# Performance work log

Hardware: AMD Instinct MI355X
Metric: run time of the kernel (lower is better)

## Reference

```python
import jax, jax.numpy as jnp
import numpy as np

C = 1.0                      # Poincare-ball curvature (m.default_c)
SQC = C ** 0.5
EPS = 1e-6


def _norm(x):
    return jnp.maximum(jnp.linalg.norm(x, axis=-1, keepdims=True), EPS)


def _artanh(x):
    return jnp.arctanh(jnp.clip(x, -1.0 + 1e-6, 1.0 - 1e-6))


def mobius_add(x, y):
    # Mobius addition in the Poincare ball of curvature C
    x2 = jnp.sum(x * x, axis=-1, keepdims=True)
    y2 = jnp.sum(y * y, axis=-1, keepdims=True)
    xy = jnp.sum(x * y, axis=-1, keepdims=True)
    num = (1 + 2 * C * xy + C * y2) * x + (1 - C * x2) * y
    den = 1 + 2 * C * xy + C * C * x2 * y2
    return num / jnp.maximum(den, EPS)


def mobius_matvec(x, W):
    # m.matmul(W, x, c): Mobius matrix-vector product, x:[B,Din], W:[Din,Dout]
    mx = x @ W
    xn = _norm(x)
    mxn = _norm(mx)
    return jnp.tanh(mxn / xn * _artanh(SQC * xn)) * mx / (mxn * SQC)


def _log0(x):
    xn = _norm(x)
    return _artanh(SQC * xn) * x / (SQC * xn)


def _exp0(v):
    vn = _norm(v)
    return jnp.tanh(SQC * vn) * v / (SQC * vn)


def m_tanh(x):
    # Mobius pointwise tanh: exp0(tanh(log0(x)))
    return _exp0(jnp.tanh(_log0(x)))


def setup_inputs() -> dict:
    key = jax.random.key(0)
    k1, k2, k3, k4 = jax.random.split(key, 4)
    B, T, E, H = 256, 128, 1024, 1024
    # small scale so points stay well inside the unit Poincare ball
    inp = jax.random.normal(k1, (B, T, E), dtype=jnp.float32) * 0.02
    W_ih = jax.random.normal(k2, (E, H), dtype=jnp.float32) * 0.02
    W_hh = jax.random.normal(k3, (H, H), dtype=jnp.float32) * 0.02
    b_h = jax.random.uniform(k4, (H,), dtype=jnp.float32, minval=-0.01, maxval=0.01)
    return {"inp": inp, "W_ih": W_ih, "W_hh": W_hh, "b_h": b_h}


def reference(inp, W_ih, W_hh, b_h):
    B, T, E = inp.shape
    H = W_hh.shape[0]
    h0 = jnp.zeros((B, H), dtype=inp.dtype)

    def step(h, xt):
        prem = mobius_matvec(xt, W_ih)                       # [B,H]
        hid = mobius_add(mobius_matvec(h, W_hh), b_h[None])  # [B,H]
        h_next = m_tanh(mobius_add(prem, hid))
        return h_next, None

    h_last, _ = jax.lax.scan(step, h0, jnp.swapaxes(inp, 0, 1))  # scan over T
    return h_last
```

## Files before the change

### kernel.cpp

```cpp
#include <hip/hip_runtime.h>

#define EPSF 1e-6f
#define ONEM 0.999999f
#define Bb 256
#define Tt 128
#define Kd 1024

typedef __attribute__((ext_vector_type(8))) short s16x8;
typedef __attribute__((ext_vector_type(4))) short s16x4;
typedef __attribute__((ext_vector_type(4))) float f32x4;
typedef unsigned long long ull;

union PF { ull u; float f[2]; };

__device__ __forceinline__ short f2bf(float f) {
  unsigned u = __float_as_uint(f);
  u += 0x7fffu + ((u >> 16) & 1u);
  return (short)(u >> 16);
}
__device__ __forceinline__ float bf2f(short s) {
  return __uint_as_float(((unsigned)(unsigned short)s) << 16);
}
__device__ __forceinline__ float ftanh(float x) {
  float e = __expf(2.f * x);
  return 1.f - 2.f / (e + 1.f);
}
__device__ __forceinline__ float fatanh(float x) {
  return 0.5f * __logf((1.f + x) / (1.f - x));
}
__device__ __forceinline__ float red16(float v) {
#pragma unroll
  for (int m = 8; m >= 1; m >>= 1) v += __shfl_xor(v, m, 64);
  return v;
}

__device__ __forceinline__ float brsum(float v) {
  __shared__ float sb[4];
#pragma unroll
  for (int m = 32; m >= 1; m >>= 1) v += __shfl_xor(v, m, 64);
  __syncthreads();
  if ((threadIdx.x & 63) == 0) sb[threadIdx.x >> 6] = v;
  __syncthreads();
  return sb[0] + sb[1] + sb[2] + sb[3];
}

__device__ __forceinline__ void gbarR(int* c) {
  __syncthreads();
  if (threadIdx.x == 0) {
    __hip_atomic_fetch_add(c, 1, __ATOMIC_RELAXED, __HIP_MEMORY_SCOPE_AGENT);
    while (__hip_atomic_load(c, __ATOMIC_RELAXED, __HIP_MEMORY_SCOPE_AGENT) < 16)
      __builtin_amdgcn_s_sleep(1);
  }
  __syncthreads();
}

__global__ void wcvt_kernel(const float* __restrict__ W, short* __restrict__ WT) {
  __shared__ float tile[64][65];
  const int k0 = blockIdx.y * 64, n0 = blockIdx.x * 64;
  const int t = threadIdx.x;
#pragma unroll
  for (int i = 0; i < 16; i++) {
    int e = i * 256 + t, r = e >> 6, c = e & 63;
    tile[r][c] = W[(k0 + r) * Kd + n0 + c];
  }
  __syncthreads();
#pragma unroll
  for (int i = 0; i < 16; i++) {
    int e = i * 256 + t, rn = e >> 6, ck = e & 63;
    WT[(n0 + rn) * Kd + k0 + ck] = f2bf(tile[ck][rn]);
  }
}

__global__ void wfrag_kernel(const float* __restrict__ W, short* __restrict__ Wf) {
  const int bid = blockIdx.x;
  const int nn = threadIdx.x & 15, kk = threadIdx.x >> 4;
  const int l = (kk >> 2) * 16 + nn;
  const int jj = (kk & 3) * 2;
  const int nt = bid >> 5, kt = bid & 31;
  const int n = nt * 16 + nn;
  const int k = kt * 32 + (kk >> 2) * 8 + jj;
  unsigned lo = (unsigned)(unsigned short)f2bf(W[(size_t)k * Kd + n]);
  unsigned hi = (unsigned)(unsigned short)f2bf(W[(size_t)(k + 1) * Kd + n]);
  ((unsigned*)Wf)[((size_t)bid * 64 + l) * 4 + (jj >> 1)] = lo | (hi << 16);
}

__global__ void icvt_kernel(const float* __restrict__ inp, short* __restrict__ out) {
  int i = blockIdx.x * 2048 + threadIdx.x * 8;
  float4 a = *(const float4*)(inp + i);
  float4 b = *(const float4*)(inp + i + 4);
  s16x8 v;
  v[0] = f2bf(a.x); v[1] = f2bf(a.y); v[2] = f2bf(a.z); v[3] = f2bf(a.w);
  v[4] = f2bf(b.x); v[5] = f2bf(b.y); v[6] = f2bf(b.z); v[7] = f2bf(b.w);
  *(s16x8*)(out + i) = v;
}

__global__ void __launch_bounds__(256) gemm_p_kernel(const short* __restrict__ A,
                                                     const short* __restrict__ BT,
                                                     short* __restrict__ C) {
  const int n0 = blockIdx.x * 64, m0 = blockIdx.y * 64;
  const int tid = threadIdx.x, w = tid >> 6, l = tid & 63, lm = l & 15, q = l >> 4;
  const short* ap = A + (m0 + w * 16 + lm) * Kd + q * 8;
  const short* bp = BT + (n0 + lm) * Kd + q * 8;
  f32x4 acc0 = {0.f, 0.f, 0.f, 0.f}, acc1 = acc0, acc2 = acc0, acc3 = acc0;
#pragma unroll 4
  for (int k = 0; k < Kd; k += 32) {
    s16x8 a = *(const s16x8*)(ap + k);
    s16x8 b0 = *(const s16x8*)(bp + k);
    s16x8 b1 = *(const s16x8*)(bp + 16 * Kd + k);
    s16x8 b2 = *(const s16x8*)(bp + 32 * Kd + k);
    s16x8 b3 = *(const s16x8*)(bp + 48 * Kd + k);
    acc0 = __builtin_amdgcn_mfma_f32_16x16x32_bf16(a, b0, acc0, 0, 0, 0);
    acc1 = __builtin_amdgcn_mfma_f32_16x16x32_bf16(a, b1, acc1, 0, 0, 0);
    acc2 = __builtin_amdgcn_mfma_f32_16x16x32_bf16(a, b2, acc2, 0, 0, 0);
    acc3 = __builtin_amdgcn_mfma_f32_16x16x32_bf16(a, b3, acc3, 0, 0, 0);
  }
  const int row = m0 + w * 16 + q * 4, col = n0 + lm;
#pragma unroll
  for (int r = 0; r < 4; r++) {
    C[(row + r) * Kd + col] = f2bf(acc0[r]);
    C[(row + r) * Kd + col + 16] = f2bf(acc1[r]);
    C[(row + r) * Kd + col + 32] = f2bf(acc2[r]);
    C[(row + r) * Kd + col + 48] = f2bf(acc3[r]);
  }
}

__global__ void __launch_bounds__(256) rowscale_kernel(const float* __restrict__ inp,
                                                       const float* __restrict__ bh,
                                                       short* __restrict__ P,
                                                       float* __restrict__ pn2,
                                                       float* __restrict__ pb2) {
  const int r = blockIdx.x, tid = threadIdx.x, i0 = tid * 4;
  float4 xv = *(const float4*)(inp + r * Kd + i0);
  float xn2 = brsum(xv.x * xv.x + xv.y * xv.y + xv.z * xv.z + xv.w * xv.w);
  s16x4 pr = *(const s16x4*)(P + r * Kd + i0);
  float p0 = bf2f(pr[0]), p1 = bf2f(pr[1]), p2 = bf2f(pr[2]), p3 = bf2f(pr[3]);
  float mxn2 = brsum(p0 * p0 + p1 * p1 + p2 * p2 + p3 * p3);
  float xn = fmaxf(sqrtf(xn2), EPSF);
  float mxn = fmaxf(sqrtf(mxn2), EPSF);
  float sc = tanhf(mxn / xn * atanhf(fminf(xn, ONEM))) / mxn;
  s16x4 po;
  po[0] = f2bf(sc * p0); po[1] = f2bf(sc * p1);
  po[2] = f2bf(sc * p2); po[3] = f2bf(sc * p3);
  *(s16x4*)(P + r * Kd + i0) = po;
  float4 bv = *(const float4*)(bh + i0);
  float s0 = bf2f(po[0]), s1 = bf2f(po[1]), s2v = bf2f(po[2]), s3 = bf2f(po[3]);
  float pn2v = brsum(s0 * s0 + s1 * s1 + s2v * s2v + s3 * s3);
  float pbv = brsum(s0 * bv.x + s1 * bv.y + s2v * bv.z + s3 * bv.w);
  if (tid == 0) { pn2[r] = pn2v; pb2[r] = pbv; }
}

__global__ void __launch_bounds__(256, 1) rnn_kernel(
    const short* __restrict__ Wf, const short* __restrict__ P,
    const float* __restrict__ pn2, const float* __restrict__ pb2,
    const float* __restrict__ bh, float* __restrict__ out,
    float* __restrict__ S, int* __restrict__ cnt, ull* __restrict__ ubuf) {
  __shared__ short us[16][1032];
  __shared__ float red[4][16][4];
  __shared__ float bex[4];
  const int tid = threadIdx.x, w = tid >> 6, l = tid & 63, lm = l & 15, q = l >> 4;
  const int g = blockIdx.x & 15, nb = blockIdx.x >> 4;
  const int gr0 = g * 16;
  const int c = nb * 64 + w * 16 + lm;
  const int nt = nb * 4 + w;

  for (int i = tid; i < 8256; i += 256) ((int*)us)[i] = 0;

  float4 bv4 = *(const float4*)(bh + tid * 4);
  float bp = bv4.x * bv4.x + bv4.y * bv4.y + bv4.z * bv4.z + bv4.w * bv4.w;
#pragma unroll
  for (int m = 32; m >= 1; m >>= 1) bp += __shfl_xor(bp, m, 64);
  if (l == 0) bex[w] = bp;
  __syncthreads();
  const float b2 = bex[0] + bex[1] + bex[2] + bex[3];
  const float bb = bh[c];

  s16x8 wfr[32];
#pragma unroll
  for (int kt = 0; kt < 32; kt++)
    wfr[kt] = *(const s16x8*)(Wf + ((size_t)(nt * 32 + kt) * 64 + l) * 8);

  const short* ar = &us[0][0] + lm * 1032 + q * 8;
  float lam[4] = {1.f, 1.f, 1.f, 1.f};
  float hn2c[4] = {0.f, 0.f, 0.f, 0.f};

  for (int t = 0; t < Tt; t++) {
    float pv[4], p2s[4], pbr[4];
#pragma unroll
    for (int r = 0; r < 4; r++) {
      size_t rt = (size_t)(gr0 + q * 4 + r) * Tt + t;
      pv[r] = bf2f(P[rt * Kd + c]);
      p2s[r] = pn2[rt];
      pbr[r] = pb2[rt];
    }

    f32x4 c0 = {0.f, 0.f, 0.f, 0.f}, c1v = c0, c2v = c0, c3v = c0;
#pragma unroll
    for (int kt = 0; kt < 32; kt += 4) {
      s16x8 a0 = *(const s16x8*)(ar + (kt + 0) * 32);
      s16x8 a1 = *(const s16x8*)(ar + (kt + 1) * 32);
      s16x8 a2 = *(const s16x8*)(ar + (kt + 2) * 32);
      s16x8 a3 = *(const s16x8*)(ar + (kt + 3) * 32);
      c0 = __builtin_amdgcn_mfma_f32_16x16x32_bf16(a0, wfr[kt], c0, 0, 0, 0);
      c1v = __builtin_amdgcn_mfma_f32_16x16x32_bf16(a1, wfr[kt + 1], c1v, 0, 0, 0);
      c2v = __builtin_amdgcn_mfma_f32_16x16x32_bf16(a2, wfr[kt + 2], c2v, 0, 0, 0);
      c3v = __builtin_amdgcn_mfma_f32_16x16x32_bf16(a3, wfr[kt + 3], c3v, 0, 0, 0);
    }
    f32x4 accv = (c0 + c1v) + (c2v + c3v);
    float mx[4];
#pragma unroll
    for (int r = 0; r < 4; r++) mx[r] = lam[r] * accv[r];

#pragma unroll
    for (int r = 0; r < 4; r++) {
      float vm2 = red16(mx[r] * mx[r]);
      float vmb = red16(mx[r] * bb);
      float vpm = red16(pv[r] * mx[r]);
      if (lm == 0) {
        red[w][q * 4 + r][0] = vm2;
        red[w][q * 4 + r][1] = vmb;
        red[w][q * 4 + r][2] = vpm;
      }
    }
    __syncthreads();
    float* Sg = S + ((size_t)t * 16 + g) * 64;
    if (tid < 64) {
      int row = tid >> 2, s = tid & 3;
      if (s < 3) {
        float v = red[0][row][s] + red[1][row][s] + red[2][row][s] + red[3][row][s];
        __hip_atomic_fetch_add(&Sg[row * 4 + s], v, __ATOMIC_RELAXED,
                               __HIP_MEMORY_SCOPE_AGENT);
      }
    }
    int* cg = cnt + ((size_t)t * 16 + g) * 16;
    gbarR(cg);

    float uu[4], u2p[4];
#pragma unroll
    for (int r = 0; r < 4; r++) {
      PF d01;
      d01.u = __hip_atomic_load((ull*)Sg + (q * 4 + r) * 2, __ATOMIC_RELAXED,
                                __HIP_MEMORY_SCOPE_AGENT);
      float Spm = __hip_atomic_load(&Sg[(q * 4 + r) * 4 + 2], __ATOMIC_RELAXED,
                                    __HIP_MEMORY_SCOPE_AGENT);
      float Smm = d01.f[0], Smb = d01.f[1];
      float hn = fmaxf(sqrtf(hn2c[r]), EPSF);
      float mxn = fmaxf(sqrtf(Smm), EPSF);
      float sc = ftanh(mxn / hn * fatanh(fminf(hn, ONEM))) / mxn;
      float x2 = sc * sc * Smm;
      float xy = sc * Smb;
      float den = fmaxf(1.f + 2.f * xy + x2 * b2, EPSF);
      float al = ((1.f + 2.f * xy + b2) / den) * sc;
      float be = (1.f - x2) / den;
      float hh2 = al * al * Smm + 2.f * al * be * Smb + be * be * b2;
      float ph = al * Spm + be * pbr[r];
      float den2 = fmaxf(1.f + 2.f * ph + p2s[r] * hh2, EPSF);
      float cc1 = (1.f + 2.f * ph + hh2) / den2;
      float cc2 = (1.f - p2s[r]) / den2;
      float z = cc1 * pv[r] + cc2 * (al * mx[r] + be * bb);
      float z2 = cc1 * cc1 * p2s[r] + cc2 * cc2 * hh2 + 2.f * cc1 * cc2 * ph;
      float zn = fmaxf(sqrtf(z2), EPSF);
      float gg = fatanh(fminf(zn, ONEM)) / zn;
      uu[r] = ftanh(gg * z);
      u2p[r] = red16(uu[r] * uu[r]);
    }

    const int p = t & 1;
    ull* ubw = ubuf + ((size_t)(p * 16 + g) * 16) * 256;
    const int ent = nb * 16 + w * 4 + (lm >> 2);
#pragma unroll
    for (int r = 0; r < 4; r++) {
      unsigned v16 = (unsigned)(unsigned short)f2bf(uu[r]);
      unsigned o1 = (unsigned)__shfl_xor((int)v16, 1, 64);
      unsigned plo = v16 | (o1 << 16);
      unsigned phi = (unsigned)__shfl_xor((int)plo, 2, 64);
      if ((lm & 3) == 0) {
        ull pk = (ull)plo | ((ull)phi << 32);
        __hip_atomic_store(&ubw[(q * 4 + r) * 256 + ent], pk, __ATOMIC_RELAXED,
                           __HIP_MEMORY_SCOPE_AGENT);
      }
      if (lm == 0) red[w][q * 4 + r][3] = u2p[r];
    }
    __syncthreads();
    if (tid < 16) {
      float v = red[0][tid][3] + red[1][tid][3] + red[2][tid][3] + red[3][tid][3];
      __hip_atomic_fetch_add(&Sg[tid * 4 + 3], v, __ATOMIC_RELAXED,
                             __HIP_MEMORY_SCOPE_AGENT);
    }
    gbarR(cg + 8);

#pragma unroll
    for (int r = 0; r < 4; r++) {
      float u2 = __hip_atomic_load(&Sg[(q * 4 + r) * 4 + 3], __ATOMIC_RELAXED,
                                   __HIP_MEMORY_SCOPE_AGENT);
      float un = fmaxf(sqrtf(u2), EPSF);
      float s2 = ftanh(un) / un;
      lam[r] = s2;
      hn2c[r] = s2 * s2 * u2;
      if (t == Tt - 1)
        out[(size_t)(gr0 + q * 4 + r) * Kd + c] = s2 * uu[r];
    }

    const ull* ub = ubuf + ((size_t)(p * 16 + g) * 16) * 256;
#pragma unroll
    for (int i = 0; i < 16; i++) {
      ull v = __hip_atomic_load(&ub[i * 256 + tid], __ATOMIC_RELAXED,
                                __HIP_MEMORY_SCOPE_AGENT);
      *(ull*)&us[i][tid * 4] = v;
    }
    __syncthreads();
  }
}

extern "C" void kernel_launch(void* const* d_in, const int* in_sizes, int n_in,
                              void* d_out, int out_size, void* d_ws, size_t ws_size,
                              hipStream_t stream) {
  const float* inp = (const float*)d_in[0];
  const float* Wih = (const float*)d_in[1];
  const float* Whh = (const float*)d_in[2];
  const float* bh = (const float*)d_in[3];

  char* ws = (char*)d_ws;
  size_t off = 0;
  float* S = (float*)(ws + off); off += (size_t)Tt * 16 * 64 * 4;
  int* cnt = (int*)(ws + off); off += (size_t)Tt * 16 * 16 * 4;
  size_t zbytes = off;
  ull* ubuf = (ull*)(ws + off); off += (size_t)2 * 16 * 16 * 256 * 8;
  float* pn2 = (float*)(ws + off); off += (size_t)Bb * Tt * 4;
  float* pb2 = (float*)(ws + off); off += (size_t)Bb * Tt * 4;
  short* WTih = (short*)(ws + off); off += (size_t)Kd * Kd * 2;
  short* Wfhh = (short*)(ws + off); off += (size_t)Kd * Kd * 2;
  short* Ab = (short*)(ws + off); off += (size_t)Bb * Tt * Kd * 2;
  short* P = (short*)(ws + off); off += (size_t)Bb * Tt * Kd * 2;

  hipMemsetAsync(d_ws, 0, zbytes, stream);

  wcvt_kernel<<<dim3(16, 16), 256, 0, stream>>>(Wih, WTih);
  wfrag_kernel<<<2048, 256, 0, stream>>>(Whh, Wfhh);
  icvt_kernel<<<(Bb * Tt * Kd) / 2048, 256, 0, stream>>>(inp, Ab);
  gemm_p_kernel<<<dim3(16, (Bb * Tt) / 64), 256, 0, stream>>>(Ab, WTih, P);
  rowscale_kernel<<<Bb * Tt, 256, 0, stream>>>(inp, bh, P, pn2, pb2);
  rnn_kernel<<<256, 256, 0, stream>>>(Wfhh, P, pn2, pb2, bh, (float*)d_out,
                                      S, cnt, ubuf);
}
```

Baseline: 2.131 ms.

## Split RNN batch into 32 groups of 8 rows and stream W_hh from global memory

The persistent recurrent kernel now uses 512 blocks, each handling 8 batch rows instead of 16, so there are 32 row groups across 16 column blocks. The 32 resident W_hh fragments are no longer kept in registers and are read from global memory (or L2) on every timestep. Launch bounds are raised to allow two blocks per CU. Only half of the MFMA tile rows are valid, so half the MMA work is duplicated and discarded. The intent is to shorten per-block barrier latency and raise parallelism, at the cost of reloading weights every step and doing redundant MMA work.

```diff
diff --git a/kernel.cpp b/kernel.cpp
--- a/kernel.cpp
+++ b/kernel.cpp
@@ -149,7 +149,7 @@
   if (tid == 0) { pn2[r] = pn2v; pb2[r] = pbv; }
 }
 
-__global__ void __launch_bounds__(256, 1) rnn_kernel(
+__global__ void __launch_bounds__(256, 2) rnn_kernel(
     const short* __restrict__ Wf, const short* __restrict__ P,
     const float* __restrict__ pn2, const float* __restrict__ pb2,
     const float* __restrict__ bh, float* __restrict__ out,
@@ -158,8 +158,8 @@
   __shared__ float red[4][16][4];
   __shared__ float bex[4];
   const int tid = threadIdx.x, w = tid >> 6, l = tid & 63, lm = l & 15, q = l >> 4;
-  const int g = blockIdx.x & 15, nb = blockIdx.x >> 4;
-  const int gr0 = g * 16;
+  const int g = blockIdx.x >> 4, nb = blockIdx.x & 15;
+  const int gr0 = g * 8;
   const int c = nb * 64 + w * 16 + lm;
   const int nt = nb * 4 + w;
 
@@ -174,12 +174,8 @@
   const float b2 = bex[0] + bex[1] + bex[2] + bex[3];
   const float bb = bh[c];
 
-  s16x8 wfr[32];
-#pragma unroll
-  for (int kt = 0; kt < 32; kt++)
-    wfr[kt] = *(const s16x8*)(Wf + ((size_t)(nt * 32 + kt) * 64 + l) * 8);
-
   const short* ar = &us[0][0] + lm * 1032 + q * 8;
+  const short* wp = Wf + (size_t)nt * 32 * 512 + l * 8;
   float lam[4] = {1.f, 1.f, 1.f, 1.f};
   float hn2c[4] = {0.f, 0.f, 0.f, 0.f};
 
@@ -187,7 +183,7 @@
     float pv[4], p2s[4], pbr[4];
 #pragma unroll
     for (int r = 0; r < 4; r++) {
-      size_t rt = (size_t)(gr0 + q * 4 + r) * Tt + t;
+      size_t rt = (size_t)(gr0 + ((q * 4 + r) & 7)) * Tt + t;
       pv[r] = bf2f(P[rt * Kd + c]);
       p2s[r] = pn2[rt];
       pbr[r] = pb2[rt];
@@ -200,10 +196,14 @@
       s16x8 a1 = *(const s16x8*)(ar + (kt + 1) * 32);
       s16x8 a2 = *(const s16x8*)(ar + (kt + 2) * 32);
       s16x8 a3 = *(const s16x8*)(ar + (kt + 3) * 32);
-      c0 = __builtin_amdgcn_mfma_f32_16x16x32_bf16(a0, wfr[kt], c0, 0, 0, 0);
-      c1v = __builtin_amdgcn_mfma_f32_16x16x32_bf16(a1, wfr[kt + 1], c1v, 0, 0, 0);
-      c2v = __builtin_amdgcn_mfma_f32_16x16x32_bf16(a2, wfr[kt + 2], c2v, 0, 0, 0);
-      c3v = __builtin_amdgcn_mfma_f32_16x16x32_bf16(a3, wfr[kt + 3], c3v, 0, 0, 0);
+      s16x8 b0 = *(const s16x8*)(wp + (size_t)(kt + 0) * 512);
+      s16x8 b1 = *(const s16x8*)(wp + (size_t)(kt + 1) * 512);
+      s16x8 b2 = *(const s16x8*)(wp + (size_t)(kt + 2) * 512);
+      s16x8 b3 = *(const s16x8*)(wp + (size_t)(kt + 3) * 512);
+      c0 = __builtin_amdgcn_mfma_f32_16x16x32_bf16(a0, b0, c0, 0, 0, 0);
+      c1v = __builtin_amdgcn_mfma_f32_16x16x32_bf16(a1, b1, c1v, 0, 0, 0);
+      c2v = __builtin_amdgcn_mfma_f32_16x16x32_bf16(a2, b2, c2v, 0, 0, 0);
+      c3v = __builtin_amdgcn_mfma_f32_16x16x32_bf16(a3, b3, c3v, 0, 0, 0);
     }
     f32x4 accv = (c0 + c1v) + (c2v + c3v);
     float mx[4];
@@ -222,8 +222,8 @@
       }
     }
     __syncthreads();
-    float* Sg = S + ((size_t)t * 16 + g) * 64;
-    if (tid < 64) {
+    float* Sg = S + ((size_t)t * 32 + g) * 32;
+    if (tid < 32) {
       int row = tid >> 2, s = tid & 3;
       if (s < 3) {
         float v = red[0][row][s] + red[1][row][s] + red[2][row][s] + red[3][row][s];
@@ -231,16 +231,17 @@
                                __HIP_MEMORY_SCOPE_AGENT);
       }
     }
-    int* cg = cnt + ((size_t)t * 16 + g) * 16;
+    int* cg = cnt + ((size_t)t * 32 + g) * 16;
     gbarR(cg);
 
     float uu[4], u2p[4];
 #pragma unroll
     for (int r = 0; r < 4; r++) {
+      int rr = (q * 4 + r) & 7;
       PF d01;
-      d01.u = __hip_atomic_load((ull*)Sg + (q * 4 + r) * 2, __ATOMIC_RELAXED,
+      d01.u = __hip_atomic_load((ull*)Sg + rr * 2, __ATOMIC_RELAXED,
                                 __HIP_MEMORY_SCOPE_AGENT);
-      float Spm = __hip_atomic_load(&Sg[(q * 4 + r) * 4 + 2], __ATOMIC_RELAXED,
+      float Spm = __hip_atomic_load(&Sg[rr * 4 + 2], __ATOMIC_RELAXED,
                                     __HIP_MEMORY_SCOPE_AGENT);
       float Smm = d01.f[0], Smb = d01.f[1];
       float hn = fmaxf(sqrtf(hn2c[r]), EPSF);
@@ -265,7 +266,7 @@
     }
 
     const int p = t & 1;
-    ull* ubw = ubuf + ((size_t)(p * 16 + g) * 16) * 256;
+    ull* ubw = ubuf + ((size_t)(p * 32 + g) * 8) * 256;
     const int ent = nb * 16 + w * 4 + (lm >> 2);
 #pragma unroll
     for (int r = 0; r < 4; r++) {
@@ -273,15 +274,15 @@
       unsigned o1 = (unsigned)__shfl_xor((int)v16, 1, 64);
       unsigned plo = v16 | (o1 << 16);
       unsigned phi = (unsigned)__shfl_xor((int)plo, 2, 64);
-      if ((lm & 3) == 0) {
+      if (q < 2 && (lm & 3) == 0) {
         ull pk = (ull)plo | ((ull)phi << 32);
         __hip_atomic_store(&ubw[(q * 4 + r) * 256 + ent], pk, __ATOMIC_RELAXED,
                            __HIP_MEMORY_SCOPE_AGENT);
       }
-      if (lm == 0) red[w][q * 4 + r][3] = u2p[r];
+      if (q < 2 && lm == 0) red[w][q * 4 + r][3] = u2p[r];
     }
     __syncthreads();
-    if (tid < 16) {
+    if (tid < 8) {
       float v = red[0][tid][3] + red[1][tid][3] + red[2][tid][3] + red[3][tid][3];
       __hip_atomic_fetch_add(&Sg[tid * 4 + 3], v, __ATOMIC_RELAXED,
                              __HIP_MEMORY_SCOPE_AGENT);
@@ -290,19 +291,20 @@
 
 #pragma unroll
     for (int r = 0; r < 4; r++) {
-      float u2 = __hip_atomic_load(&Sg[(q * 4 + r) * 4 + 3], __ATOMIC_RELAXED,
+      int rr = (q * 4 + r) & 7;
+      float u2 = __hip_atomic_load(&Sg[rr * 4 + 3], __ATOMIC_RELAXED,
                                    __HIP_MEMORY_SCOPE_AGENT);
       float un = fmaxf(sqrtf(u2), EPSF);
       float s2 = ftanh(un) / un;
       lam[r] = s2;
       hn2c[r] = s2 * s2 * u2;
-      if (t == Tt - 1)
+      if (q < 2 && t == Tt - 1)
         out[(size_t)(gr0 + q * 4 + r) * Kd + c] = s2 * uu[r];
     }
 
-    const ull* ub = ubuf + ((size_t)(p * 16 + g) * 16) * 256;
-#pragma unroll
-    for (int i = 0; i < 16; i++) {
+    const ull* ub = ubuf + ((size_t)(p * 32 + g) * 8) * 256;
+#pragma unroll
+    for (int i = 0; i < 8; i++) {
       ull v = __hip_atomic_load(&ub[i * 256 + tid], __ATOMIC_RELAXED,
                                 __HIP_MEMORY_SCOPE_AGENT);
       *(ull*)&us[i][tid * 4] = v;
@@ -321,10 +323,10 @@
 
   char* ws = (char*)d_ws;
   size_t off = 0;
-  float* S = (float*)(ws + off); off += (size_t)Tt * 16 * 64 * 4;
-  int* cnt = (int*)(ws + off); off += (size_t)Tt * 16 * 16 * 4;
+  float* S = (float*)(ws + off); off += (size_t)Tt * 32 * 32 * 4;
+  int* cnt = (int*)(ws + off); off += (size_t)Tt * 32 * 16 * 4;
   size_t zbytes = off;
-  ull* ubuf = (ull*)(ws + off); off += (size_t)2 * 16 * 16 * 256 * 8;
+  ull* ubuf = (ull*)(ws + off); off += (size_t)2 * 32 * 8 * 256 * 8;
   float* pn2 = (float*)(ws + off); off += (size_t)Bb * Tt * 4;
   float* pb2 = (float*)(ws + off); off += (size_t)Bb * Tt * 4;
   short* WTih = (short*)(ws + off); off += (size_t)Kd * Kd * 2;
@@ -339,6 +341,6 @@
   icvt_kernel<<<(Bb * Tt * Kd) / 2048, 256, 0, stream>>>(inp, Ab);
   gemm_p_kernel<<<dim3(16, (Bb * Tt) / 64), 256, 0, stream>>>(Ab, WTih, P);
   rowscale_kernel<<<Bb * Tt, 256, 0, stream>>>(inp, bh, P, pn2, pb2);
-  rnn_kernel<<<256, 256, 0, stream>>>(Wfhh, P, pn2, pb2, bh, (float*)d_out,
+  rnn_kernel<<<512, 256, 0, stream>>>(Wfhh, P, pn2, pb2, bh, (float*)d_out,
                                       S, cnt, ubuf);
 }
```

Result: slower. 2.463 ms (+15.6%).
